# Optimization experiments

Measured on AMD Instinct MI355X. Metric: run time of the kernel, lower is better.

The kernel has to match this reference:

```python
import jax, jax.numpy as jnp
import numpy as np

N = 50000       # nodes
E = 800000      # edges
IN = 128        # in_channels
H = 8           # heads
C = 32          # out_channels per head
HC = H * C      # 256
NEG_SLOPE = 0.2


def setup_inputs() -> dict:
    key = jax.random.key(0)
    ks = jax.random.split(key, 8)
    s_in = 1.0 / np.sqrt(IN)
    s_c = 1.0 / np.sqrt(C)
    x = jax.random.normal(ks[0], (N, IN), dtype=jnp.float32)
    edge_index = jax.random.randint(ks[1], (2, E), 0, N, dtype=jnp.int64)
    W_l = jax.random.normal(ks[2], (IN, HC), dtype=jnp.float32) * s_in   # lin_l weight
    W_r = jax.random.normal(ks[3], (IN, HC), dtype=jnp.float32) * s_in   # lin_r weight
    att = jax.random.normal(ks[4], (H, C), dtype=jnp.float32) * s_c      # attention vector a
    bias = jax.random.normal(ks[5], (HC,), dtype=jnp.float32) * 0.02
    Wp = jax.random.normal(ks[6], (IN, HC), dtype=jnp.float32) * s_in    # residual proj weight
    bp = jax.random.normal(ks[7], (HC,), dtype=jnp.float32) * 0.02
    return {"x": x, "edge_index": edge_index, "W_l": W_l, "W_r": W_r,
            "att": att, "bias": bias, "Wp": Wp, "bp": bp}


def _gatv2_forward(x, edge_index, W_l, W_r, att, bias, Wp, bp):
    src = edge_index[0]  # source j (message sender)
    dst = edge_index[1]  # target i (softmax segment)
    xl = (x @ W_l).reshape(N, H, C)  # messages / left branch
    xr = (x @ W_r).reshape(N, H, C)  # right (target) branch
    # per-edge GATv2 score: a^T LeakyReLU(xl_j + xr_i)
    e = xl[src] + xr[dst]                              # [E, H, C]
    e = jnp.where(e >= 0, e, NEG_SLOPE * e)            # LeakyReLU(0.2)
    score = jnp.einsum('ehc,hc->eh', e, att)           # [E, H]
    # segment softmax over incoming edges of each target node
    m = jax.ops.segment_max(score, dst, num_segments=N)   # [N, H]
    m = jnp.where(jnp.isfinite(m), m, 0.0)                 # empty segments -> 0
    ex = jnp.exp(score - m[dst])                            # [E, H]
    denom = jax.ops.segment_sum(ex, dst, num_segments=N)   # [N, H]
    alpha = ex / jnp.maximum(denom[dst], 1e-16)             # [E, H]
    # scatter-aggregate alpha-weighted source messages
    msg = alpha[:, :, None] * xl[src]                       # [E, H, C]
    out = jax.ops.segment_sum(msg, dst, num_segments=N)    # [N, H, C]
    out = out.reshape(N, HC) + bias
    # residual projection + GELU (exact erf, like torch F.gelu default)
    res = x @ Wp + bp
    return jax.nn.gelu(out + res, approximate=False)


def reference(x, edge_index, W_l, W_r, att, bias, Wp, bp):
    return _gatv2_forward(x, edge_index, W_l, W_r, att, bias, Wp, bp)
```

## Files before the change

### kernel.cpp

```cpp
#include <hip/hip_runtime.h>
#include <math.h>

#define N_NODES 50000
#define N_EDGES 800000
#define K_IN    128
#define HC      256
#define NCOLS   768

typedef __bf16 bf16x8 __attribute__((ext_vector_type(8)));
typedef float  f32x4  __attribute__((ext_vector_type(4)));

__device__ inline ushort f32_to_bf16(float f)
{
    union { float f; uint u; } c; c.f = f;
    uint r = c.u + 0x7fff + ((c.u >> 16) & 1);
    return (ushort)(r >> 16);
}
__device__ inline float bf16_to_f32(ushort u)
{
    union { uint u; float f; } c; c.u = (uint)u << 16;
    return c.f;
}
__device__ inline float4 bf4_to_f4(uint2 u)
{
    float4 r;
    r.x = __uint_as_float(u.x << 16);
    r.y = __uint_as_float(u.x & 0xffff0000u);
    r.z = __uint_as_float(u.y << 16);
    r.w = __uint_as_float(u.y & 0xffff0000u);
    return r;
}

__global__ void convert_w_kernel(const float* __restrict__ Wl,
                                 const float* __restrict__ Wr,
                                 const float* __restrict__ Wp,
                                 ushort* __restrict__ Wt_hi,
                                 ushort* __restrict__ Wt_lo)
{
    int t = blockIdx.x * 256 + threadIdx.x;
    if (t >= NCOLS * K_IN) return;
    int n = t >> 7, k = t & 127;
    const float* W = (n < 256) ? Wl : (n < 512) ? Wr : Wp;
    int nn = n & 255;
    float v = W[(size_t)k * HC + nn];
    ushort h = f32_to_bf16(v);
    Wt_hi[t] = h;
    Wt_lo[t] = f32_to_bf16(v - bf16_to_f32(h));
}

__global__ __launch_bounds__(256, 2) void gemm_mfma_kernel(
    const float* __restrict__ x,
    const ushort* __restrict__ Wt_hi, const ushort* __restrict__ Wt_lo,
    const float* __restrict__ bp,
    ushort* __restrict__ xfb, float* __restrict__ res)
{
    __shared__ ushort Ah[128 * 64], Al[128 * 64], Bh[128 * 64], Bl[128 * 64];

    const int bm = blockIdx.x;
    const int bn = blockIdx.y;
    const int nbase = bn * 128;
    const int tid = threadIdx.x;
    const int lane = tid & 63;
    const int w = tid >> 6;
    const int wr = w >> 1, wc = w & 1;
    const int fr = lane & 15;
    const int kg = lane >> 4;

    f32x4 acc[4][4];
#pragma unroll
    for (int mi = 0; mi < 4; ++mi)
#pragma unroll
        for (int ni = 0; ni < 4; ++ni) acc[mi][ni] = (f32x4)0.f;

#pragma unroll
    for (int ks = 0; ks < 2; ++ks) {
        const int k0 = ks * 64;
#pragma unroll
        for (int i = 0; i < 8; ++i) {
            int f = tid + i * 256;
            int r = f >> 4, q = f & 15;
            int grow = bm * 128 + r;
            float4 v = make_float4(0.f, 0.f, 0.f, 0.f);
            if (grow < N_NODES)
                v = *reinterpret_cast<const float4*>(&x[(size_t)grow * K_IN + k0 + q * 4]);
            ushort h0 = f32_to_bf16(v.x), h1 = f32_to_bf16(v.y);
            ushort h2 = f32_to_bf16(v.z), h3 = f32_to_bf16(v.w);
            ushort l0 = f32_to_bf16(v.x - bf16_to_f32(h0));
            ushort l1 = f32_to_bf16(v.y - bf16_to_f32(h1));
            ushort l2 = f32_to_bf16(v.z - bf16_to_f32(h2));
            ushort l3 = f32_to_bf16(v.w - bf16_to_f32(h3));
            int off = r * 64 + ((q * 4) ^ ((r & 7) << 3));
            uint2 hp = make_uint2((uint)h0 | ((uint)h1 << 16), (uint)h2 | ((uint)h3 << 16));
            uint2 lp = make_uint2((uint)l0 | ((uint)l1 << 16), (uint)l2 | ((uint)l3 << 16));
            *reinterpret_cast<uint2*>(&Ah[off]) = hp;
            *reinterpret_cast<uint2*>(&Al[off]) = lp;
        }
#pragma unroll
        for (int i = 0; i < 8; ++i) {
            int f = tid + i * 256;
            int n = f >> 4, q = f & 15;
            size_t g = (size_t)(nbase + n) * K_IN + k0 + q * 4;
            uint2 hv = *reinterpret_cast<const uint2*>(&Wt_hi[g]);
            uint2 lv = *reinterpret_cast<const uint2*>(&Wt_lo[g]);
            int off = n * 64 + ((q * 4) ^ ((n & 7) << 3));
            *reinterpret_cast<uint2*>(&Bh[off]) = hv;
            *reinterpret_cast<uint2*>(&Bl[off]) = lv;
        }
        __syncthreads();
#pragma unroll
        for (int kk = 0; kk < 2; ++kk) {
            const int kush = kk * 32 + kg * 8;
            bf16x8 ah[4], al[4], bh[4], blo[4];
#pragma unroll
            for (int mi = 0; mi < 4; ++mi) {
                int row = wr * 64 + mi * 16 + fr;
                int off = row * 64 + (kush ^ ((row & 7) << 3));
                ah[mi] = *reinterpret_cast<const bf16x8*>(&Ah[off]);
                al[mi] = *reinterpret_cast<const bf16x8*>(&Al[off]);
            }
#pragma unroll
            for (int ni = 0; ni < 4; ++ni) {
                int nrow = wc * 64 + ni * 16 + fr;
                int off = nrow * 64 + (kush ^ ((nrow & 7) << 3));
                bh[ni]  = *reinterpret_cast<const bf16x8*>(&Bh[off]);
                blo[ni] = *reinterpret_cast<const bf16x8*>(&Bl[off]);
            }
#pragma unroll
            for (int mi = 0; mi < 4; ++mi)
#pragma unroll
                for (int ni = 0; ni < 4; ++ni) {
                    acc[mi][ni] = __builtin_amdgcn_mfma_f32_16x16x32_bf16(ah[mi], bh[ni],  acc[mi][ni], 0, 0, 0);
                    acc[mi][ni] = __builtin_amdgcn_mfma_f32_16x16x32_bf16(al[mi], bh[ni],  acc[mi][ni], 0, 0, 0);
                    acc[mi][ni] = __builtin_amdgcn_mfma_f32_16x16x32_bf16(ah[mi], blo[ni], acc[mi][ni], 0, 0, 0);
                }
        }
        __syncthreads();
    }

    if (bn < 4) {
#pragma unroll
        for (int mi = 0; mi < 4; ++mi)
#pragma unroll
            for (int i = 0; i < 4; ++i) {
                int row = bm * 128 + wr * 64 + mi * 16 + kg * 4 + i;
                if (row >= N_NODES) continue;
#pragma unroll
                for (int ni = 0; ni < 4; ++ni) {
                    int col = nbase + wc * 64 + ni * 16 + fr;
                    xfb[(size_t)row * 512 + col] = f32_to_bf16(acc[mi][ni][i]);
                }
            }
    } else {
        float badd[4];
#pragma unroll
        for (int ni = 0; ni < 4; ++ni)
            badd[ni] = bp[nbase - 512 + wc * 64 + ni * 16 + fr];
#pragma unroll
        for (int mi = 0; mi < 4; ++mi)
#pragma unroll
            for (int i = 0; i < 4; ++i) {
                int row = bm * 128 + wr * 64 + mi * 16 + kg * 4 + i;
                if (row >= N_NODES) continue;
#pragma unroll
                for (int ni = 0; ni < 4; ++ni) {
                    int col = nbase - 512 + wc * 64 + ni * 16 + fr;
                    res[(size_t)row * 256 + col] = acc[mi][ni][i] + badd[ni];
                }
            }
    }
}

#define SCAN_CH 1024
#define SCAN_NB ((N_NODES + SCAN_CH - 1) / SCAN_CH)

__global__ void zero_int_kernel(int* __restrict__ p, int n)
{
    int i = blockIdx.x * blockDim.x + threadIdx.x;
    if (i < n) p[i] = 0;
}

__global__ void hist_kernel(const int* __restrict__ ei, int* __restrict__ deg)
{
    int e = blockIdx.x * blockDim.x + threadIdx.x;
    if (e < N_EDGES) atomicAdd(&deg[ei[N_EDGES + e]], 1);
}

__device__ inline int wave_incl_scan(int v, int lane)
{
#pragma unroll
    for (int off = 1; off < 64; off <<= 1) {
        int t = __shfl_up(v, off, 64);
        if (lane >= off) v += t;
    }
    return v;
}

__device__ inline int wave_sum(int v)
{
#pragma unroll
    for (int off = 1; off < 64; off <<= 1) v += __shfl_xor(v, off, 64);
    return v;
}

__global__ __launch_bounds__(1024) void scan_partial_kernel(
    const int* __restrict__ deg, int* __restrict__ bsum)
{
    __shared__ int wsum[16];
    int i = blockIdx.x * SCAN_CH + threadIdx.x;
    int lane = threadIdx.x & 63, wid = threadIdx.x >> 6;
    int v = (i < N_NODES) ? deg[i] : 0;
    int s = wave_sum(v);
    if (lane == 0) wsum[wid] = s;
    __syncthreads();
    if (threadIdx.x == 0) {
        int t = 0;
#pragma unroll
        for (int k = 0; k < 16; ++k) t += wsum[k];
        bsum[blockIdx.x] = t;
    }
}

__global__ void scan_base_kernel(const int* __restrict__ bsum,
                                 int* __restrict__ bbase, int* __restrict__ offs)
{
    int lane = threadIdx.x;
    int v = (lane < SCAN_NB) ? bsum[lane] : 0;
    int inc = wave_incl_scan(v, lane);
    if (lane < SCAN_NB) bbase[lane] = inc - v;
    if (lane == 63) offs[N_NODES] = inc;
}

__global__ __launch_bounds__(1024) void scan_final_kernel(
    const int* __restrict__ deg, const int* __restrict__ bbase,
    int* __restrict__ offs, int* __restrict__ cursor)
{
    __shared__ int wsum[16];
    int i = blockIdx.x * SCAN_CH + threadIdx.x;
    int lane = threadIdx.x & 63, wid = threadIdx.x >> 6;
    int v = (i < N_NODES) ? deg[i] : 0;
    int inc = wave_incl_scan(v, lane);
    if (lane == 63) wsum[wid] = inc;
    __syncthreads();
    if (wid == 0) {
        int wv = (lane < 16) ? wsum[lane] : 0;
        int ws = wave_incl_scan(wv, lane);
        if (lane < 16) wsum[lane] = ws;
    }
    __syncthreads();
    int wbase = wid ? wsum[wid - 1] : 0;
    int excl = bbase[blockIdx.x] + wbase + inc - v;
    if (i < N_NODES) { offs[i] = excl; cursor[i] = excl; }
}

__global__ void scatter_kernel(const int* __restrict__ ei,
                               int* __restrict__ cursor, int* __restrict__ csr)
{
    int e = blockIdx.x * blockDim.x + threadIdx.x;
    if (e < N_EDGES) {
        int s = ei[e];
        int d = ei[N_EDGES + e];
        int pos = atomicAdd(&cursor[d], 1);
        csr[pos] = s;
    }
}

__device__ inline float edge_score(float4 v, float4 xrv, float4 attv)
{
    float tx = v.x + xrv.x, ty = v.y + xrv.y, tz = v.z + xrv.z, tw = v.w + xrv.w;
    tx = fmaxf(tx, 0.f) + 0.2f * fminf(tx, 0.f);
    ty = fmaxf(ty, 0.f) + 0.2f * fminf(ty, 0.f);
    tz = fmaxf(tz, 0.f) + 0.2f * fminf(tz, 0.f);
    tw = fmaxf(tw, 0.f) + 0.2f * fminf(tw, 0.f);
    float p = attv.x * tx + attv.y * ty + attv.z * tz + attv.w * tw;
    p += __shfl_xor(p, 1, 64);
    p += __shfl_xor(p, 2, 64);
    p += __shfl_xor(p, 4, 64);
    return p;
}

__global__ __launch_bounds__(256) void gat_agg_kernel(
    const ushort* __restrict__ xfb, const float* __restrict__ res,
    const int* __restrict__ offs, const int* __restrict__ csr,
    const float* __restrict__ att, const float* __restrict__ bias,
    float* __restrict__ out)
{
    const int lane = threadIdx.x & 63;
    const int wid = threadIdx.x >> 6;
    const int node = blockIdx.x * 4 + wid;
    if (node >= N_NODES) return;

    const uint2* __restrict__ xfb2 = reinterpret_cast<const uint2*>(xfb);
    const float4 attv = reinterpret_cast<const float4*>(att)[lane];
    const float4 xrv = bf4_to_f4(xfb2[(size_t)node * 128 + 64 + lane]);

    const int e0 = offs[node];
    const int e1 = offs[node + 1];

    float m = -INFINITY, d = 0.f;
    float4 acc = make_float4(0.f, 0.f, 0.f, 0.f);

    int e = e0;
    for (; e + 1 < e1; e += 2) {
        int s0 = csr[e];
        int s1 = csr[e + 1];
        float4 v0 = bf4_to_f4(xfb2[(size_t)s0 * 128 + lane]);
        float4 v1 = bf4_to_f4(xfb2[(size_t)s1 * 128 + lane]);
        float p0 = edge_score(v0, xrv, attv);
        float p1 = edge_score(v1, xrv, attv);
        float mnew = fmaxf(m, fmaxf(p0, p1));
        float scale = __expf(m - mnew);
        float w0 = __expf(p0 - mnew);
        float w1 = __expf(p1 - mnew);
        d = d * scale + w0 + w1;
        acc.x = acc.x * scale + w0 * v0.x + w1 * v1.x;
        acc.y = acc.y * scale + w0 * v0.y + w1 * v1.y;
        acc.z = acc.z * scale + w0 * v0.z + w1 * v1.z;
        acc.w = acc.w * scale + w0 * v0.w + w1 * v1.w;
        m = mnew;
    }
    if (e < e1) {
        int s0 = csr[e];
        float4 v0 = bf4_to_f4(xfb2[(size_t)s0 * 128 + lane]);
        float p0 = edge_score(v0, xrv, attv);
        float mnew = fmaxf(m, p0);
        float scale = __expf(m - mnew);
        float w0 = __expf(p0 - mnew);
        d = d * scale + w0;
        acc.x = acc.x * scale + w0 * v0.x;
        acc.y = acc.y * scale + w0 * v0.y;
        acc.z = acc.z * scale + w0 * v0.z;
        acc.w = acc.w * scale + w0 * v0.w;
        m = mnew;
    }

    float inv = 1.f / fmaxf(d, 1e-16f);
    const float4 bv = reinterpret_cast<const float4*>(bias)[lane];
    const float4 rv = reinterpret_cast<const float4*>(res)[(size_t)node * 64 + lane];
    float4 o;
    o.x = acc.x * inv + bv.x + rv.x;
    o.y = acc.y * inv + bv.y + rv.y;
    o.z = acc.z * inv + bv.z + rv.z;
    o.w = acc.w * inv + bv.w + rv.w;
    o.x = 0.5f * o.x * (1.f + erff(o.x * 0.70710678118654752f));
    o.y = 0.5f * o.y * (1.f + erff(o.y * 0.70710678118654752f));
    o.z = 0.5f * o.z * (1.f + erff(o.z * 0.70710678118654752f));
    o.w = 0.5f * o.w * (1.f + erff(o.w * 0.70710678118654752f));
    reinterpret_cast<float4*>(out)[(size_t)node * 64 + lane] = o;
}

extern "C" void kernel_launch(void* const* d_in, const int* in_sizes, int n_in,
                              void* d_out, int out_size, void* d_ws, size_t ws_size,
                              hipStream_t stream)
{
    const float* x    = (const float*)d_in[0];
    const int*   ei   = (const int*)d_in[1];
    const float* Wl   = (const float*)d_in[2];
    const float* Wr   = (const float*)d_in[3];
    const float* att  = (const float*)d_in[4];
    const float* bias = (const float*)d_in[5];
    const float* Wp   = (const float*)d_in[6];
    const float* bp   = (const float*)d_in[7];
    float* out = (float*)d_out;

    ushort* xfb   = (ushort*)d_ws;
    float*  res   = (float*)(xfb + (size_t)N_NODES * 512);
    ushort* Wt_hi = (ushort*)(res + (size_t)N_NODES * 256);
    ushort* Wt_lo = Wt_hi + NCOLS * K_IN;
    int* deg    = (int*)(Wt_lo + NCOLS * K_IN);
    int* offs   = deg + N_NODES;
    int* cursor = offs + N_NODES + 1;
    int* csr    = cursor + N_NODES;
    int* bsum   = csr + N_EDGES;
    int* bbase  = bsum + SCAN_NB;

    hipLaunchKernelGGL(convert_w_kernel, dim3((NCOLS * K_IN + 255) / 256), dim3(256), 0, stream,
                       Wl, Wr, Wp, Wt_hi, Wt_lo);
    hipLaunchKernelGGL(zero_int_kernel, dim3((N_NODES + 255) / 256), dim3(256), 0, stream,
                       deg, N_NODES);
    hipLaunchKernelGGL(hist_kernel, dim3((N_EDGES + 255) / 256), dim3(256), 0, stream,
                       ei, deg);
    hipLaunchKernelGGL(scan_partial_kernel, dim3(SCAN_NB), dim3(1024), 0, stream,
                       deg, bsum);
    hipLaunchKernelGGL(scan_base_kernel, dim3(1), dim3(64), 0, stream,
                       bsum, bbase, offs);
    hipLaunchKernelGGL(scan_final_kernel, dim3(SCAN_NB), dim3(1024), 0, stream,
                       deg, bbase, offs, cursor);
    hipLaunchKernelGGL(scatter_kernel, dim3((N_EDGES + 255) / 256), dim3(256), 0, stream,
                       ei, cursor, csr);
    hipLaunchKernelGGL(gemm_mfma_kernel, dim3((N_NODES + 127) / 128, 6), dim3(256), 0, stream,
                       x, Wt_hi, Wt_lo, bp, xfb, res);
    hipLaunchKernelGGL(gat_agg_kernel, dim3((N_NODES + 3) / 4), dim3(256), 0, stream,
                       xfb, res, offs, csr, att, bias, out);
}
```

Before: 331.2 us.

## Precompute x bf16 split, simplify LeakyReLU score, drop online-max rescaling in aggregation

Adds a separate kernel that splits x into bf16 hi/lo halves once, so the six N-tile GEMM blocks no longer each redo the conversion. In the aggregation kernel, LeakyReLU is rewritten as 0.6*x+0.4*|x| folded into the attention weights. The running softmax max is replaced by a fixed reference taken from the first edge's score, which removes the per-step rescale exp. The edge loop is unrolled by four and indexing is switched to 32-bit. The fixed reference can overflow exp if later scores are much larger than the first, and the extra kernel adds a round trip of x through memory.

```diff
diff --git a/kernel.cpp b/kernel.cpp
--- a/kernel.cpp
+++ b/kernel.cpp
@@ -29,6 +29,24 @@
     r.z = __uint_as_float(u.y << 16);
     r.w = __uint_as_float(u.y & 0xffff0000u);
     return r;
+}
+
+__global__ void convert_x_kernel(const float* __restrict__ x,
+                                 ushort* __restrict__ Xh, ushort* __restrict__ Xl)
+{
+    int t = blockIdx.x * 256 + threadIdx.x;
+    if (t >= N_NODES * (K_IN / 4)) return;
+    float4 v = reinterpret_cast<const float4*>(x)[t];
+    ushort h0 = f32_to_bf16(v.x), h1 = f32_to_bf16(v.y);
+    ushort h2 = f32_to_bf16(v.z), h3 = f32_to_bf16(v.w);
+    ushort l0 = f32_to_bf16(v.x - bf16_to_f32(h0));
+    ushort l1 = f32_to_bf16(v.y - bf16_to_f32(h1));
+    ushort l2 = f32_to_bf16(v.z - bf16_to_f32(h2));
+    ushort l3 = f32_to_bf16(v.w - bf16_to_f32(h3));
+    reinterpret_cast<uint2*>(Xh)[t] =
+        make_uint2((uint)h0 | ((uint)h1 << 16), (uint)h2 | ((uint)h3 << 16));
+    reinterpret_cast<uint2*>(Xl)[t] =
+        make_uint2((uint)l0 | ((uint)l1 << 16), (uint)l2 | ((uint)l3 << 16));
 }
 
 __global__ void convert_w_kernel(const float* __restrict__ Wl,
@@ -49,7 +67,7 @@
 }
 
 __global__ __launch_bounds__(256, 2) void gemm_mfma_kernel(
-    const float* __restrict__ x,
+    const ushort* __restrict__ Xh, const ushort* __restrict__ Xl,
     const ushort* __restrict__ Wt_hi, const ushort* __restrict__ Wt_lo,
     const float* __restrict__ bp,
     ushort* __restrict__ xfb, float* __restrict__ res)
@@ -80,20 +98,15 @@
             int f = tid + i * 256;
             int r = f >> 4, q = f & 15;
             int grow = bm * 128 + r;
-            float4 v = make_float4(0.f, 0.f, 0.f, 0.f);
-            if (grow < N_NODES)
-                v = *reinterpret_cast<const float4*>(&x[(size_t)grow * K_IN + k0 + q * 4]);
-            ushort h0 = f32_to_bf16(v.x), h1 = f32_to_bf16(v.y);
-            ushort h2 = f32_to_bf16(v.z), h3 = f32_to_bf16(v.w);
-            ushort l0 = f32_to_bf16(v.x - bf16_to_f32(h0));
-            ushort l1 = f32_to_bf16(v.y - bf16_to_f32(h1));
-            ushort l2 = f32_to_bf16(v.z - bf16_to_f32(h2));
-            ushort l3 = f32_to_bf16(v.w - bf16_to_f32(h3));
+            uint2 hv = make_uint2(0u, 0u), lv = make_uint2(0u, 0u);
+            if (grow < N_NODES) {
+                size_t g = (size_t)grow * K_IN + k0 + q * 4;
+                hv = *reinterpret_cast<const uint2*>(&Xh[g]);
+                lv = *reinterpret_cast<const uint2*>(&Xl[g]);
+            }
             int off = r * 64 + ((q * 4) ^ ((r & 7) << 3));
-            uint2 hp = make_uint2((uint)h0 | ((uint)h1 << 16), (uint)h2 | ((uint)h3 << 16));
-            uint2 lp = make_uint2((uint)l0 | ((uint)l1 << 16), (uint)l2 | ((uint)l3 << 16));
-            *reinterpret_cast<uint2*>(&Ah[off]) = hp;
-            *reinterpret_cast<uint2*>(&Al[off]) = lp;
+            *reinterpret_cast<uint2*>(&Ah[off]) = hv;
+            *reinterpret_cast<uint2*>(&Al[off]) = lv;
         }
 #pragma unroll
         for (int i = 0; i < 8; ++i) {
@@ -264,14 +277,13 @@
     }
 }
 
-__device__ inline float edge_score(float4 v, float4 xrv, float4 attv)
-{
-    float tx = v.x + xrv.x, ty = v.y + xrv.y, tz = v.z + xrv.z, tw = v.w + xrv.w;
-    tx = fmaxf(tx, 0.f) + 0.2f * fminf(tx, 0.f);
-    ty = fmaxf(ty, 0.f) + 0.2f * fminf(ty, 0.f);
-    tz = fmaxf(tz, 0.f) + 0.2f * fminf(tz, 0.f);
-    tw = fmaxf(tw, 0.f) + 0.2f * fminf(tw, 0.f);
-    float p = attv.x * tx + attv.y * ty + attv.z * tz + attv.w * tw;
+__device__ inline float escore(float4 v, float4 xrv, float4 a1, float4 a2)
+{
+    float x0 = v.x + xrv.x, x1 = v.y + xrv.y, x2 = v.z + xrv.z, x3 = v.w + xrv.w;
+    float p = a1.x * x0 + a2.x * fabsf(x0);
+    p = fmaf(a1.y, x1, p); p = fmaf(a2.y, fabsf(x1), p);
+    p = fmaf(a1.z, x2, p); p = fmaf(a2.z, fabsf(x2), p);
+    p = fmaf(a1.w, x3, p); p = fmaf(a2.w, fabsf(x3), p);
     p += __shfl_xor(p, 1, 64);
     p += __shfl_xor(p, 2, 64);
     p += __shfl_xor(p, 4, 64);
@@ -291,51 +303,59 @@
 
     const uint2* __restrict__ xfb2 = reinterpret_cast<const uint2*>(xfb);
     const float4 attv = reinterpret_cast<const float4*>(att)[lane];
-    const float4 xrv = bf4_to_f4(xfb2[(size_t)node * 128 + 64 + lane]);
+    float4 a1, a2;
+    a1.x = 0.6f * attv.x; a1.y = 0.6f * attv.y; a1.z = 0.6f * attv.z; a1.w = 0.6f * attv.w;
+    a2.x = 0.4f * attv.x; a2.y = 0.4f * attv.y; a2.z = 0.4f * attv.z; a2.w = 0.4f * attv.w;
+    const float4 xrv = bf4_to_f4(xfb2[(uint)node * 128u + 64u + lane]);
 
     const int e0 = offs[node];
     const int e1 = offs[node + 1];
 
-    float m = -INFINITY, d = 0.f;
+    float m = 0.f, d = 0.f;
     float4 acc = make_float4(0.f, 0.f, 0.f, 0.f);
 
     int e = e0;
-    for (; e + 1 < e1; e += 2) {
+    if (e < e1) {
+        int s = csr[e];
+        float4 v = bf4_to_f4(xfb2[((uint)s << 7) + lane]);
+        m = escore(v, xrv, a1, a2);
+        d = 1.f;
+        acc = v;
+        ++e;
+    }
+    for (; e + 3 < e1; e += 4) {
+        int s0 = csr[e], s1 = csr[e + 1], s2 = csr[e + 2], s3 = csr[e + 3];
+        float4 v0 = bf4_to_f4(xfb2[((uint)s0 << 7) + lane]);
+        float4 v1 = bf4_to_f4(xfb2[((uint)s1 << 7) + lane]);
+        float4 v2 = bf4_to_f4(xfb2[((uint)s2 << 7) + lane]);
+        float4 v3 = bf4_to_f4(xfb2[((uint)s3 << 7) + lane]);
+        float p0 = escore(v0, xrv, a1, a2);
+        float p1 = escore(v1, xrv, a1, a2);
+        float p2 = escore(v2, xrv, a1, a2);
+        float p3 = escore(v3, xrv, a1, a2);
+        float w0 = __expf(p0 - m), w1 = __expf(p1 - m);
+        float w2 = __expf(p2 - m), w3 = __expf(p3 - m);
+        d += (w0 + w1) + (w2 + w3);
+        acc.x = fmaf(w3, v3.x, fmaf(w2, v2.x, fmaf(w1, v1.x, fmaf(w0, v0.x, acc.x))));
+        acc.y = fmaf(w3, v3.y, fmaf(w2, v2.y, fmaf(w1, v1.y, fmaf(w0, v0.y, acc.y))));
+        acc.z = fmaf(w3, v3.z, fmaf(w2, v2.z, fmaf(w1, v1.z, fmaf(w0, v0.z, acc.z))));
+        acc.w = fmaf(w3, v3.w, fmaf(w2, v2.w, fmaf(w1, v1.w, fmaf(w0, v0.w, acc.w))));
+    }
+    for (; e < e1; ++e) {
         int s0 = csr[e];
-        int s1 = csr[e + 1];
-        float4 v0 = bf4_to_f4(xfb2[(size_t)s0 * 128 + lane]);
-        float4 v1 = bf4_to_f4(xfb2[(size_t)s1 * 128 + lane]);
-        float p0 = edge_score(v0, xrv, attv);
-        float p1 = edge_score(v1, xrv, attv);
-        float mnew = fmaxf(m, fmaxf(p0, p1));
-        float scale = __expf(m - mnew);
-        float w0 = __expf(p0 - mnew);
-        float w1 = __expf(p1 - mnew);
-        d = d * scale + w0 + w1;
-        acc.x = acc.x * scale + w0 * v0.x + w1 * v1.x;
-        acc.y = acc.y * scale + w0 * v0.y + w1 * v1.y;
-        acc.z = acc.z * scale + w0 * v0.z + w1 * v1.z;
-        acc.w = acc.w * scale + w0 * v0.w + w1 * v1.w;
-        m = mnew;
-    }
-    if (e < e1) {
-        int s0 = csr[e];
-        float4 v0 = bf4_to_f4(xfb2[(size_t)s0 * 128 + lane]);
-        float p0 = edge_score(v0, xrv, attv);
-        float mnew = fmaxf(m, p0);
-        float scale = __expf(m - mnew);
-        float w0 = __expf(p0 - mnew);
-        d = d * scale + w0;
-        acc.x = acc.x * scale + w0 * v0.x;
-        acc.y = acc.y * scale + w0 * v0.y;
-        acc.z = acc.z * scale + w0 * v0.z;
-        acc.w = acc.w * scale + w0 * v0.w;
-        m = mnew;
+        float4 v0 = bf4_to_f4(xfb2[((uint)s0 << 7) + lane]);
+        float p0 = escore(v0, xrv, a1, a2);
+        float w0 = __expf(p0 - m);
+        d += w0;
+        acc.x = fmaf(w0, v0.x, acc.x);
+        acc.y = fmaf(w0, v0.y, acc.y);
+        acc.z = fmaf(w0, v0.z, acc.z);
+        acc.w = fmaf(w0, v0.w, acc.w);
     }
 
     float inv = 1.f / fmaxf(d, 1e-16f);
     const float4 bv = reinterpret_cast<const float4*>(bias)[lane];
-    const float4 rv = reinterpret_cast<const float4*>(res)[(size_t)node * 64 + lane];
+    const float4 rv = reinterpret_cast<const float4*>(res)[(uint)node * 64u + lane];
     float4 o;
     o.x = acc.x * inv + bv.x + rv.x;
     o.y = acc.y * inv + bv.y + rv.y;
@@ -345,7 +365,7 @@
     o.y = 0.5f * o.y * (1.f + erff(o.y * 0.70710678118654752f));
     o.z = 0.5f * o.z * (1.f + erff(o.z * 0.70710678118654752f));
     o.w = 0.5f * o.w * (1.f + erff(o.w * 0.70710678118654752f));
-    reinterpret_cast<float4*>(out)[(size_t)node * 64 + lane] = o;
+    reinterpret_cast<float4*>(out)[(uint)node * 64u + lane] = o;
 }
 
 extern "C" void kernel_launch(void* const* d_in, const int* in_sizes, int n_in,
@@ -364,7 +384,9 @@
 
     ushort* xfb   = (ushort*)d_ws;
     float*  res   = (float*)(xfb + (size_t)N_NODES * 512);
-    ushort* Wt_hi = (ushort*)(res + (size_t)N_NODES * 256);
+    ushort* Xh    = (ushort*)(res + (size_t)N_NODES * 256);
+    ushort* Xl    = Xh + (size_t)N_NODES * K_IN;
+    ushort* Wt_hi = Xl + (size_t)N_NODES * K_IN;
     ushort* Wt_lo = Wt_hi + NCOLS * K_IN;
     int* deg    = (int*)(Wt_lo + NCOLS * K_IN);
     int* offs   = deg + N_NODES;
@@ -373,6 +395,8 @@
     int* bsum   = csr + N_EDGES;
     int* bbase  = bsum + SCAN_NB;
 
+    hipLaunchKernelGGL(convert_x_kernel, dim3((N_NODES * (K_IN / 4) + 255) / 256), dim3(256), 0, stream,
+                       x, Xh, Xl);
     hipLaunchKernelGGL(convert_w_kernel, dim3((NCOLS * K_IN + 255) / 256), dim3(256), 0, stream,
                        Wl, Wr, Wp, Wt_hi, Wt_lo);
     hipLaunchKernelGGL(zero_int_kernel, dim3((N_NODES + 255) / 256), dim3(256), 0, stream,
@@ -388,7 +412,7 @@
     hipLaunchKernelGGL(scatter_kernel, dim3((N_EDGES + 255) / 256), dim3(256), 0, stream,
                        ei, cursor, csr);
     hipLaunchKernelGGL(gemm_mfma_kernel, dim3((N_NODES + 127) / 128, 6), dim3(256), 0, stream,
-                       x, Wt_hi, Wt_lo, bp, xfb, res);
+                       Xh, Xl, Wt_hi, Wt_lo, bp, xfb, res);
     hipLaunchKernelGGL(gat_agg_kernel, dim3((N_NODES + 3) / 4), dim3(256), 0, stream,
                        xfb, res, offs, csr, att, bias, out);
 }
```

Measured after the change: 325.7 us. About the same (-1.7%).
